# Performance work log

Hardware: AMD Instinct MI355X
Metric: run time of the kernel (lower is better)

The kernel has to match this reference:

```python
import jax, jax.numpy as jnp
import numpy as np

B, N, K, F, OUT = 32, 2000, 32, 64, 128

def setup_inputs() -> dict:
    key = jax.random.key(0)
    k1, k2, k3, k4, k5 = jax.random.split(key, 5)
    x = jax.random.normal(k1, (B, N, F), dtype=jnp.float32)
    neighborhood = jax.random.randint(k2, (N, K), 0, N, dtype=jnp.int64)
    distances = jax.random.uniform(k3, (N, K), dtype=jnp.float32)
    # Linear(k*(F+1), OUT): torch default init scale ~ 1/sqrt(fan_in)
    fan_in = K * (F + 1)
    W = jax.random.normal(k4, (OUT, fan_in), dtype=jnp.float32) / np.sqrt(fan_in)
    b = jax.random.normal(k5, (OUT,), dtype=jnp.float32) / np.sqrt(fan_in)
    return {"x": x, "neighborhood": neighborhood, "distances": distances, "W": W, "b": b}

def reference(x, neighborhood, distances, W, b):
    batch, seq_len, feat = x.shape          # [B, N, F]
    k = neighborhood.shape[1]
    gathered = x[:, neighborhood, :]        # [B, N, K, F] gather over sequence dim
    d = jnp.broadcast_to(distances[None, :, :, None], (batch, seq_len, k, 1))
    h = jnp.concatenate([gathered, d], axis=-1)        # [B, N, K, F+1]
    h = h.reshape(batch, seq_len, k * (feat + 1))      # [B, N, K*(F+1)]
    out = jnp.einsum('bnf,of->bno', h, W) + b          # [B, N, OUT]
    return out
```

## Files before the change

kernel.cpp:

```cpp
#include <hip/hip_runtime.h>
#include <hip/hip_bf16.h>
#include <stdint.h>

typedef __attribute__((ext_vector_type(8)))  __bf16   bf16x8;
typedef __attribute__((ext_vector_type(16))) float    f32x16;
typedef __attribute__((ext_vector_type(8)))  float    f32x8;

#define NB   32
#define NN   2000
#define NK   32
#define NF   64
#define NOUT 128
#define NSTEP 130

#define GLOBAL_AS __attribute__((address_space(1)))
#define LDS_AS    __attribute__((address_space(3)))
#define SB() __builtin_amdgcn_sched_barrier(0)
#define MFMA __builtin_amdgcn_mfma_f32_32x32x16_bf16

__global__ void kprep(const float* __restrict__ x, const float* __restrict__ dist,
                      const float* __restrict__ W,
                      __bf16* __restrict__ xb2, __bf16* __restrict__ db,
                      __bf16* __restrict__ Wf) {
  const int t = threadIdx.x;
  if (blockIdx.x < NN) {
    __shared__ __bf16 sm[32 * 66];
    const int n = blockIdx.x;
    const int bb = t >> 3;
    const int f0 = (t & 7) << 3;
    const float* src = x + ((size_t)bb * NN + n) * NF + f0;
    f32x8 v = *(const f32x8*)src;
    bf16x8 r;
#pragma unroll
    for (int j = 0; j < 8; ++j) r[j] = (__bf16)v[j];
    *(bf16x8*)&sm[bb * 66 + f0] = r;
    __syncthreads();
    const int col = t & 31, half = (t >> 5) & 1, s = t >> 6;
    bf16x8 o = *(const bf16x8*)&sm[col * 66 + s * 16 + half * 8];
    *(bf16x8*)((char*)xb2 + ((size_t)n << 12) + t * 16) = o;
    if (t < NK) db[n * NK + t] = (__bf16)dist[n * NK + t];
  } else {
    const int kstep = blockIdx.x - NN;
    const int lane = t & 63;
    const int wv = t >> 6;
    const int o = wv * 32 + (lane & 31);
    const int kbase = kstep * 16 + (lane >> 5) * 8;
    bf16x8 r;
#pragma unroll
    for (int j = 0; j < 8; ++j) {
      const int kg = kbase + j;
      const int c = (kg < 2048) ? ((kg >> 6) * 65 + (kg & 63)) : ((kg - 2048) * 65 + 64);
      r[j] = (__bf16)W[(size_t)o * 2080 + c];
    }
    *(bf16x8*)(Wf + (((size_t)kstep * 256 + t) << 3)) = r;
  }
}

__global__ __launch_bounds__(256, 2) void kmain(
    const int* __restrict__ nbrs, const float* __restrict__ bias,
    const __bf16* __restrict__ xb2, const __bf16* __restrict__ Wf,
    const __bf16* __restrict__ db, float* __restrict__ out) {
  __shared__ __align__(16) char lds[2][32768];

  const int t    = threadIdx.x;
  const int lane = t & 63;
  const int w    = t >> 6;
  const int col  = lane & 31;
  const int half = lane >> 5;
  const int n0   = blockIdx.x * 4;
  const int n    = n0 + w;

  f32x16 acc0 = {}, acc1 = {}, acc2 = {}, acc3 = {};

  int myidx = 0;
  if (lane < NK) myidx = nbrs[n * NK + lane];

  auto loadA = [&](bf16x8* A, int c) {
#pragma unroll
    for (int p = 0; p < 2; ++p) {
      const int nb = __builtin_amdgcn_readlane(myidx, c * 2 + p);
      const char* g = (const char*)xb2 + ((size_t)nb << 12) + lane * 16;
#pragma unroll
      for (int s = 0; s < 4; ++s)
        A[p * 4 + s] = *(const bf16x8*)(g + (s << 10));
    }
  };

  auto stageB = [&](int c) {
    const char* g = (const char*)Wf + ((size_t)c << 15) + (w << 10) + lane * 16;
    char* l = &lds[c & 1][w << 10];
#pragma unroll
    for (int q = 0; q < 8; ++q)
      __builtin_amdgcn_global_load_lds(
          (const GLOBAL_AS uint32_t*)(g + (q << 12)),
          (LDS_AS uint32_t*)(l + (q << 12)), 16, 0, 0);
  };

  auto compute = [&](int c, const bf16x8* A) {
    const char* lb = &lds[c & 1][0] + lane * 16;
    __builtin_amdgcn_s_setprio(1);
#pragma unroll
    for (int ks = 0; ks < 8; ++ks) {
      bf16x8 b0 = *(const bf16x8*)(lb + (ks << 12));
      bf16x8 b1 = *(const bf16x8*)(lb + (ks << 12) + 1024);
      bf16x8 b2 = *(const bf16x8*)(lb + (ks << 12) + 2048);
      bf16x8 b3 = *(const bf16x8*)(lb + (ks << 12) + 3072);
      acc0 = MFMA(A[ks], b0, acc0, 0, 0, 0);
      acc1 = MFMA(A[ks], b1, acc1, 0, 0, 0);
      acc2 = MFMA(A[ks], b2, acc2, 0, 0, 0);
      acc3 = MFMA(A[ks], b3, acc3, 0, 0, 0);
    }
    __builtin_amdgcn_s_setprio(0);
  };

  bf16x8 AA[8], AB[8];

  loadA(AA, 0); SB();
  stageB(0); SB();

#define BODY(C, AC, AL)                                     \
  loadA(AL, (C) + 1); SB();                                 \
  asm volatile("s_waitcnt vmcnt(8)" ::: "memory");          \
  __builtin_amdgcn_s_barrier(); SB();                       \
  compute((C), AC); SB();                                   \
  stageB((C) + 1); SB();

  for (int c = 0; c < 14; c += 2) {
    BODY(c + 0, AA, AB)
    BODY(c + 1, AB, AA)
  }
#undef BODY
  loadA(AB, 15); SB();
  asm volatile("s_waitcnt vmcnt(8)" ::: "memory");
  __builtin_amdgcn_s_barrier(); SB();
  compute(14, AA); SB();
  stageB(15); SB();
  asm volatile("s_waitcnt vmcnt(0)" ::: "memory");
  __builtin_amdgcn_s_barrier(); SB();
  compute(15, AB);

#pragma unroll
  for (int s = 0; s < 2; ++s) {
    const char* wt = (const char*)Wf + ((size_t)(128 + s) << 12) + lane * 16;
    bf16x8 dv = *(const bf16x8*)((const char*)db + (size_t)n * 64 + s * 32 + half * 16);
    bf16x8 b0 = *(const bf16x8*)(wt);
    bf16x8 b1 = *(const bf16x8*)(wt + 1024);
    bf16x8 b2 = *(const bf16x8*)(wt + 2048);
    bf16x8 b3 = *(const bf16x8*)(wt + 3072);
    acc0 = MFMA(dv, b0, acc0, 0, 0, 0);
    acc1 = MFMA(dv, b1, acc1, 0, 0, 0);
    acc2 = MFMA(dv, b2, acc2, 0, 0, 0);
    acc3 = MFMA(dv, b3, acc3, 0, 0, 0);
  }

  const float bv0 = bias[col], bv1 = bias[col + 32], bv2 = bias[col + 64], bv3 = bias[col + 96];
#pragma unroll
  for (int r = 0; r < 16; ++r) {
    const int row = (r & 3) + 8 * (r >> 2) + 4 * half;
    float* op = out + ((size_t)row * NN + n) * NOUT + col;
    op[0]  = acc0[r] + bv0;
    op[32] = acc1[r] + bv1;
    op[64] = acc2[r] + bv2;
    op[96] = acc3[r] + bv3;
  }
}

extern "C" void kernel_launch(void* const* d_in, const int* in_sizes, int n_in,
                              void* d_out, int out_size, void* d_ws, size_t ws_size,
                              hipStream_t stream) {
  const float* x    = (const float*)d_in[0];
  const int*   nbrs = (const int*)d_in[1];
  const float* dist = (const float*)d_in[2];
  const float* W    = (const float*)d_in[3];
  const float* bias = (const float*)d_in[4];
  float* out = (float*)d_out;

  char* ws = (char*)d_ws;
  __bf16* xb2 = (__bf16*)(ws);
  __bf16* Wf  = (__bf16*)(ws + 8192000);
  __bf16* db  = (__bf16*)(ws + 8192000 + 532480);

  kprep<<<NN + NSTEP, 256, 0, stream>>>(x, dist, W, xb2, db, Wf);
  kmain<<<NN / 4, 256, 0, stream>>>(nbrs, bias, xb2, Wf, db, out);
}
```

Measured before the change: 54.93 us.

## Switch to 16x16x32 MFMA with batch-half split and two nodes per wave

Replaces the 32x32x16 MFMA tiling with 16x16x32 MFMA. The batch is split into two halves across blocks, and each wave now handles two sequence positions, so every B fragment read from LDS feeds two MFMAs. The prep kernel writes x in a per-half layout without an LDS transpose and packs W for the new fragment shape. LDS staging per step is halved and the pipeline runs 32 smaller steps. The intent is to reuse W fragments across positions and lower LDS traffic per MFMA, at the cost of more loop iterations and smaller MFMA tiles.

```diff
diff --git a/kernel.cpp b/kernel.cpp
--- a/kernel.cpp
+++ b/kernel.cpp
@@ -3,165 +3,157 @@
 #include <stdint.h>
 
 typedef __attribute__((ext_vector_type(8)))  __bf16   bf16x8;
-typedef __attribute__((ext_vector_type(16))) float    f32x16;
+typedef __attribute__((ext_vector_type(4)))  float    f32x4;
 typedef __attribute__((ext_vector_type(8)))  float    f32x8;
 
-#define NB   32
 #define NN   2000
 #define NK   32
-#define NF   64
 #define NOUT 128
-#define NSTEP 130
 
 #define GLOBAL_AS __attribute__((address_space(1)))
 #define LDS_AS    __attribute__((address_space(3)))
 #define SB() __builtin_amdgcn_sched_barrier(0)
-#define MFMA __builtin_amdgcn_mfma_f32_32x32x16_bf16
+#define MFMA16 __builtin_amdgcn_mfma_f32_16x16x32_bf16
 
 __global__ void kprep(const float* __restrict__ x, const float* __restrict__ dist,
                       const float* __restrict__ W,
-                      __bf16* __restrict__ xb2, __bf16* __restrict__ db,
-                      __bf16* __restrict__ Wf) {
+                      __bf16* __restrict__ xb2h, __bf16* __restrict__ db,
+                      __bf16* __restrict__ Wf2) {
   const int t = threadIdx.x;
   if (blockIdx.x < NN) {
-    __shared__ __bf16 sm[32 * 66];
     const int n = blockIdx.x;
-    const int bb = t >> 3;
+    const int b  = t >> 3;
     const int f0 = (t & 7) << 3;
-    const float* src = x + ((size_t)bb * NN + n) * NF + f0;
+    const float* src = x + ((size_t)b * NN + n) * 64 + f0;
     f32x8 v = *(const f32x8*)src;
     bf16x8 r;
 #pragma unroll
     for (int j = 0; j < 8; ++j) r[j] = (__bf16)v[j];
-    *(bf16x8*)&sm[bb * 66 + f0] = r;
-    __syncthreads();
-    const int col = t & 31, half = (t >> 5) & 1, s = t >> 6;
-    bf16x8 o = *(const bf16x8*)&sm[col * 66 + s * 16 + half * 8];
-    *(bf16x8*)((char*)xb2 + ((size_t)n << 12) + t * 16) = o;
+    const int h = b >> 4, row = b & 15;
+    const int off = ((f0 >> 5) << 10) + (((((f0 >> 3) & 3) << 4) + row) << 4);
+    *(bf16x8*)((char*)xb2h + ((size_t)(h * NN + n) << 11) + off) = r;
     if (t < NK) db[n * NK + t] = (__bf16)dist[n * NK + t];
   } else {
     const int kstep = blockIdx.x - NN;
-    const int lane = t & 63;
-    const int wv = t >> 6;
-    const int o = wv * 32 + (lane & 31);
-    const int kbase = kstep * 16 + (lane >> 5) * 8;
-    bf16x8 r;
 #pragma unroll
-    for (int j = 0; j < 8; ++j) {
-      const int kg = kbase + j;
-      const int c = (kg < 2048) ? ((kg >> 6) * 65 + (kg & 63)) : ((kg - 2048) * 65 + 64);
-      r[j] = (__bf16)W[(size_t)o * 2080 + c];
+    for (int pass = 0; pass < 2; ++pass) {
+      const int it = t + pass * 256;
+      const int og = it >> 6, lane = it & 63;
+      const int o  = og * 16 + (lane & 15);
+      const int kb = kstep * 32 + ((lane >> 4) << 3);
+      bf16x8 r;
+#pragma unroll
+      for (int j = 0; j < 8; ++j) {
+        const int kg = kb + j;
+        const int col = (kg < 2048) ? ((kg >> 6) * 65 + (kg & 63)) : ((kg - 2048) * 65 + 64);
+        r[j] = (__bf16)W[(size_t)o * 2080 + col];
+      }
+      *(bf16x8*)((char*)Wf2 + (size_t)kstep * 8192 + og * 1024 + lane * 16) = r;
     }
-    *(bf16x8*)(Wf + (((size_t)kstep * 256 + t) << 3)) = r;
   }
 }
 
 __global__ __launch_bounds__(256, 2) void kmain(
     const int* __restrict__ nbrs, const float* __restrict__ bias,
-    const __bf16* __restrict__ xb2, const __bf16* __restrict__ Wf,
+    const __bf16* __restrict__ xb2h, const __bf16* __restrict__ Wf2,
     const __bf16* __restrict__ db, float* __restrict__ out) {
-  __shared__ __align__(16) char lds[2][32768];
+  __shared__ __align__(16) char lds[2][16384];
 
   const int t    = threadIdx.x;
   const int lane = t & 63;
   const int w    = t >> 6;
-  const int col  = lane & 31;
-  const int half = lane >> 5;
-  const int n0   = blockIdx.x * 4;
-  const int n    = n0 + w;
+  const int h    = blockIdx.x & 1;
+  const int n0   = (blockIdx.x >> 1) * 8 + w * 2;
+  const int colo = lane & 15;
+  const int rgrp = lane >> 4;
 
-  f32x16 acc0 = {}, acc1 = {}, acc2 = {}, acc3 = {};
+  f32x4 acc[2][8] = {};
 
-  int myidx = 0;
-  if (lane < NK) myidx = nbrs[n * NK + lane];
+  const int myidx = nbrs[(n0 + (lane >> 5)) * NK + (lane & 31)];
 
-  auto loadA = [&](bf16x8* A, int c) {
+  const char* xb = (const char*)xb2h + ((size_t)(h * NN) << 11);
+  const char* wf = (const char*)Wf2;
+
+  auto loadA = [&](bf16x8 (*A)[2], int c) {
 #pragma unroll
-    for (int p = 0; p < 2; ++p) {
-      const int nb = __builtin_amdgcn_readlane(myidx, c * 2 + p);
-      const char* g = (const char*)xb2 + ((size_t)nb << 12) + lane * 16;
-#pragma unroll
-      for (int s = 0; s < 4; ++s)
-        A[p * 4 + s] = *(const bf16x8*)(g + (s << 10));
+    for (int np = 0; np < 2; ++np) {
+      const int nb = __builtin_amdgcn_readlane(myidx, np * 32 + c);
+      const char* g = xb + ((size_t)nb << 11) + lane * 16;
+      A[np][0] = *(const bf16x8*)(g);
+      A[np][1] = *(const bf16x8*)(g + 1024);
     }
   };
 
   auto stageB = [&](int c) {
-    const char* g = (const char*)Wf + ((size_t)c << 15) + (w << 10) + lane * 16;
-    char* l = &lds[c & 1][w << 10];
+    const char* g = wf + ((size_t)c << 14) + (w << 12) + lane * 16;
+    char* l = &lds[c & 1][w << 12];
 #pragma unroll
-    for (int q = 0; q < 8; ++q)
+    for (int q = 0; q < 4; ++q)
       __builtin_amdgcn_global_load_lds(
-          (const GLOBAL_AS uint32_t*)(g + (q << 12)),
-          (LDS_AS uint32_t*)(l + (q << 12)), 16, 0, 0);
+          (const GLOBAL_AS uint32_t*)(g + (q << 10)),
+          (LDS_AS uint32_t*)(l + (q << 10)), 16, 0, 0);
   };
 
-  auto compute = [&](int c, const bf16x8* A) {
-    const char* lb = &lds[c & 1][0] + lane * 16;
+  auto compute = [&](int c, bf16x8 (*A)[2]) {
+    const char* lb = &lds[c & 1][lane * 16];
     __builtin_amdgcn_s_setprio(1);
 #pragma unroll
-    for (int ks = 0; ks < 8; ++ks) {
-      bf16x8 b0 = *(const bf16x8*)(lb + (ks << 12));
-      bf16x8 b1 = *(const bf16x8*)(lb + (ks << 12) + 1024);
-      bf16x8 b2 = *(const bf16x8*)(lb + (ks << 12) + 2048);
-      bf16x8 b3 = *(const bf16x8*)(lb + (ks << 12) + 3072);
-      acc0 = MFMA(A[ks], b0, acc0, 0, 0, 0);
-      acc1 = MFMA(A[ks], b1, acc1, 0, 0, 0);
-      acc2 = MFMA(A[ks], b2, acc2, 0, 0, 0);
-      acc3 = MFMA(A[ks], b3, acc3, 0, 0, 0);
+    for (int ks = 0; ks < 2; ++ks) {
+#pragma unroll
+      for (int og = 0; og < 8; ++og) {
+        bf16x8 bf = *(const bf16x8*)(lb + (ks << 13) + (og << 10));
+        acc[0][og] = MFMA16(A[0][ks], bf, acc[0][og], 0, 0, 0);
+        acc[1][og] = MFMA16(A[1][ks], bf, acc[1][og], 0, 0, 0);
+      }
     }
     __builtin_amdgcn_s_setprio(0);
   };
 
-  bf16x8 AA[8], AB[8];
+  bf16x8 A0[2][2], A1[2][2];
 
-  loadA(AA, 0); SB();
+  loadA(A0, 0); SB();
   stageB(0); SB();
 
 #define BODY(C, AC, AL)                                     \
   loadA(AL, (C) + 1); SB();                                 \
-  asm volatile("s_waitcnt vmcnt(8)" ::: "memory");          \
+  asm volatile("s_waitcnt vmcnt(4)" ::: "memory");          \
   __builtin_amdgcn_s_barrier(); SB();                       \
   compute((C), AC); SB();                                   \
   stageB((C) + 1); SB();
 
-  for (int c = 0; c < 14; c += 2) {
-    BODY(c + 0, AA, AB)
-    BODY(c + 1, AB, AA)
+  for (int c = 0; c < 30; c += 2) {
+    BODY(c + 0, A0, A1)
+    BODY(c + 1, A1, A0)
   }
+  BODY(30, A0, A1)
 #undef BODY
-  loadA(AB, 15); SB();
-  asm volatile("s_waitcnt vmcnt(8)" ::: "memory");
-  __builtin_amdgcn_s_barrier(); SB();
-  compute(14, AA); SB();
-  stageB(15); SB();
   asm volatile("s_waitcnt vmcnt(0)" ::: "memory");
   __builtin_amdgcn_s_barrier(); SB();
-  compute(15, AB);
+  compute(31, A1);
+
+  {
+    const char* wt = wf + ((size_t)64 << 13) + lane * 16;
+    bf16x8 d0 = *(const bf16x8*)((const char*)db + (size_t)(n0 + 0) * 64 + (rgrp << 4));
+    bf16x8 d1 = *(const bf16x8*)((const char*)db + (size_t)(n0 + 1) * 64 + (rgrp << 4));
+#pragma unroll
+    for (int og = 0; og < 8; ++og) {
+      bf16x8 bf = *(const bf16x8*)(wt + (og << 10));
+      acc[0][og] = MFMA16(d0, bf, acc[0][og], 0, 0, 0);
+      acc[1][og] = MFMA16(d1, bf, acc[1][og], 0, 0, 0);
+    }
+  }
 
 #pragma unroll
-  for (int s = 0; s < 2; ++s) {
-    const char* wt = (const char*)Wf + ((size_t)(128 + s) << 12) + lane * 16;
-    bf16x8 dv = *(const bf16x8*)((const char*)db + (size_t)n * 64 + s * 32 + half * 16);
-    bf16x8 b0 = *(const bf16x8*)(wt);
-    bf16x8 b1 = *(const bf16x8*)(wt + 1024);
-    bf16x8 b2 = *(const bf16x8*)(wt + 2048);
-    bf16x8 b3 = *(const bf16x8*)(wt + 3072);
-    acc0 = MFMA(dv, b0, acc0, 0, 0, 0);
-    acc1 = MFMA(dv, b1, acc1, 0, 0, 0);
-    acc2 = MFMA(dv, b2, acc2, 0, 0, 0);
-    acc3 = MFMA(dv, b3, acc3, 0, 0, 0);
-  }
-
-  const float bv0 = bias[col], bv1 = bias[col + 32], bv2 = bias[col + 64], bv3 = bias[col + 96];
+  for (int og = 0; og < 8; ++og) {
+    const int o = (og << 4) + colo;
+    const float bv = bias[o];
 #pragma unroll
-  for (int r = 0; r < 16; ++r) {
-    const int row = (r & 3) + 8 * (r >> 2) + 4 * half;
-    float* op = out + ((size_t)row * NN + n) * NOUT + col;
-    op[0]  = acc0[r] + bv0;
-    op[32] = acc1[r] + bv1;
-    op[64] = acc2[r] + bv2;
-    op[96] = acc3[r] + bv3;
+    for (int r = 0; r < 4; ++r) {
+      const int b = (h << 4) + (rgrp << 2) + r;
+      float* op = out + ((size_t)b * NN + n0) * NOUT + o;
+      op[0]    = acc[0][og][r] + bv;
+      op[NOUT] = acc[1][og][r] + bv;
+    }
   }
 }
 
@@ -176,10 +168,10 @@
   float* out = (float*)d_out;
 
   char* ws = (char*)d_ws;
-  __bf16* xb2 = (__bf16*)(ws);
-  __bf16* Wf  = (__bf16*)(ws + 8192000);
-  __bf16* db  = (__bf16*)(ws + 8192000 + 532480);
+  __bf16* xb2h = (__bf16*)(ws);
+  __bf16* Wf2  = (__bf16*)(ws + 8192000);
+  __bf16* db   = (__bf16*)(ws + 8192000 + 532480);
 
-  kprep<<<NN + NSTEP, 256, 0, stream>>>(x, dist, W, xb2, db, Wf);
-  kmain<<<NN / 4, 256, 0, stream>>>(nbrs, bias, xb2, Wf, db, out);
+  kprep<<<NN + 65, 256, 0, stream>>>(x, dist, W, xb2h, db, Wf2);
+  kmain<<<(NN / 8) * 2, 256, 0, stream>>>(nbrs, bias, xb2h, Wf2, db, out);
 }
```

After: 53.75 us. -2.1%, faster.
